# Optimization experiments

Hardware: AMD Instinct MI355X
Metric: run time of the kernel (lower is better)

The kernel has to match this reference:

```python
import jax, jax.numpy as jnp
import numpy as np

D = 512       # d_model
H = 8         # n_heads per pathway MHA
CTX_H = 2     # router context_attention heads
P = 16        # num_attention_pathways
K = 8         # top_k_pathways
B = 8
S = 1024
TEMP = 1.0
RH1, RH2 = 128, 64  # router hidden sizes


def mha(x, in_w, in_b, out_w, out_b, n_heads):
    """torch.nn.MultiheadAttention (batch_first, eval mode, no mask)."""
    b, s, d = x.shape
    dh = d // n_heads
    qkv = x @ in_w.T + in_b                      # [b,s,3d]
    q, k, v = jnp.split(qkv, 3, axis=-1)
    sh = lambda t: t.reshape(b, s, n_heads, dh).transpose(0, 2, 1, 3)
    q, k, v = sh(q), sh(k), sh(v)
    scale = 1.0 / float(np.sqrt(dh))
    attn = jax.nn.softmax(jnp.einsum('bhqd,bhkd->bhqk', q, k) * scale, axis=-1)
    o = jnp.einsum('bhqk,bhkd->bhqd', attn, v).transpose(0, 2, 1, 3).reshape(b, s, d)
    return o @ out_w.T + out_b


def setup_inputs() -> dict:
    key = jax.random.key(0)
    ks = jax.random.split(key, 16)
    w = 0.05  # weight init scale to keep attention logits sane
    return {
        'x': jax.random.normal(ks[0], (B, S, D), jnp.float32),
        'ctx_in_w': jax.random.normal(ks[1], (3 * D, D), jnp.float32) * w,
        'ctx_in_b': jnp.zeros((3 * D,), jnp.float32),
        'ctx_out_w': jax.random.normal(ks[2], (D, D), jnp.float32) * w,
        'ctx_out_b': jnp.zeros((D,), jnp.float32),
        'r_w1': jax.random.normal(ks[3], (RH1, D), jnp.float32) * w,
        'r_b1': jnp.zeros((RH1,), jnp.float32),
        'r_w2': jax.random.normal(ks[4], (RH2, RH1), jnp.float32) * w,
        'r_b2': jnp.zeros((RH2,), jnp.float32),
        'r_w3': jax.random.normal(ks[5], (P, RH2), jnp.float32) * w,
        'r_b3': jnp.zeros((P,), jnp.float32),
        'p_in_w': jax.random.normal(ks[6], (P, 3 * D, D), jnp.float32) * w,
        'p_in_b': jnp.zeros((P, 3 * D), jnp.float32),
        'p_out_w': jax.random.normal(ks[7], (P, D, D), jnp.float32) * w,
        'p_out_b': jnp.zeros((P, D), jnp.float32),
    }


def reference(x, ctx_in_w, ctx_in_b, ctx_out_w, ctx_out_b,
              r_w1, r_b1, r_w2, r_b2, r_w3, r_b3,
              p_in_w, p_in_b, p_out_w, p_out_b):
    b, s, d = x.shape
    # --- SemanticPathwayRouter ---
    attended = mha(x, ctx_in_w, ctx_in_b, ctx_out_w, ctx_out_b, CTX_H)
    h = jax.nn.relu(attended @ r_w1.T + r_b1)
    h = jax.nn.relu(h @ r_w2.T + r_b2)
    pathway_scores = h @ r_w3.T + r_b3            # [b,s,P]
    # --- GLBL load-balance loss (eval: no buffer updates) ---
    probs_lb = jax.nn.softmax(pathway_scores, axis=-1)
    freq = probs_lb.mean(axis=(0, 1))             # [P] (frequencies == avg scores)
    glbl_loss = P * jnp.sum(freq * freq)
    # --- top-k gating: softmax -> topk scatter -> renormalize ---
    probs = jax.nn.softmax(pathway_scores / TEMP, axis=-1)
    top_v, top_i = jax.lax.top_k(probs, K)        # [b,s,K]
    bi = jnp.arange(b)[:, None, None]
    si = jnp.arange(s)[None, :, None]
    weights = jnp.zeros_like(probs).at[bi, si, top_i].set(top_v)
    weights = weights / (weights.sum(axis=-1, keepdims=True) + 1e-8)
    # --- combine: weighted sum of P full-MHA experts (scan keeps memory low) ---
    wp = jnp.moveaxis(weights, -1, 0)             # [P,b,s]
    def step(acc, params):
        iw, ib, ow, ob, wk = params
        return acc + mha(x, iw, ib, ow, ob, H) * wk[..., None], None
    output, _ = jax.lax.scan(step, jnp.zeros_like(x),
                             (p_in_w, p_in_b, p_out_w, p_out_b, wp))
    return output, glbl_loss, weights
```

## Files before the change

### kernel.cpp

```cpp
#include <hip/hip_runtime.h>
#include <math.h>

#define TOKENS 8192
#define DM 512
#define TD 1536
#define SEQ 1024
#define NPATH 16
#define TOPK 8

typedef __bf16 bf16x8v __attribute__((ext_vector_type(8)));
typedef __bf16 bf16x4v __attribute__((ext_vector_type(4)));
typedef float f32x4v __attribute__((ext_vector_type(4)));

__device__ __forceinline__ void gload_lds16(const void* gp, unsigned lds_byte_off) {
    __builtin_amdgcn_global_load_lds(
        (const __attribute__((address_space(1))) unsigned int*)(uintptr_t)gp,
        (__attribute__((address_space(3))) unsigned int*)(uintptr_t)lds_byte_off,
        16, 0, 0);
}

__global__ __launch_bounds__(256)
void gemm_f32_nt(const float* __restrict__ A, const float* __restrict__ B,
                 const float* __restrict__ bias, float* __restrict__ C,
                 int M, int N, int K, int lda, int ldb, int ldc,
                 float alpha, int relu, int zmode)
{
    __shared__ float As[16][132];
    __shared__ float Bs[16][132];
    if (zmode == 1) {
        const int z = blockIdx.z, bb = z >> 1, hh = z & 1;
        A += (size_t)bb * SEQ * TD + hh * 256;
        B += (size_t)bb * SEQ * TD + 512 + hh * 256;
        C += (size_t)z * SEQ * SEQ;
    }
    const int tid = threadIdx.x;
    const int bm = blockIdx.y << 7, bn = blockIdx.x << 7;
    const int tx4 = (tid & 15) << 2, ty4 = ((tid >> 4) & 15) << 2;
    float acc[8][8] = {};
    for (int k0 = 0; k0 < K; k0 += 16) {
        __syncthreads();
#pragma unroll
        for (int it = 0; it < 2; ++it) {
            const int u = (it << 8) + tid;
            const int row = u >> 2, kc4 = (u & 3) << 2;
            const float4 av = *(const float4*)(A + (size_t)(bm + row) * lda + k0 + kc4);
            As[kc4 + 0][row] = av.x; As[kc4 + 1][row] = av.y;
            As[kc4 + 2][row] = av.z; As[kc4 + 3][row] = av.w;
            const float4 bv = *(const float4*)(B + (size_t)(bn + row) * ldb + k0 + kc4);
            Bs[kc4 + 0][row] = bv.x; Bs[kc4 + 1][row] = bv.y;
            Bs[kc4 + 2][row] = bv.z; Bs[kc4 + 3][row] = bv.w;
        }
        __syncthreads();
#pragma unroll
        for (int kk = 0; kk < 16; ++kk) {
            const float4 a0 = *(const float4*)&As[kk][ty4];
            const float4 a1 = *(const float4*)&As[kk][64 + ty4];
            const float4 b0 = *(const float4*)&Bs[kk][tx4];
            const float4 b1 = *(const float4*)&Bs[kk][64 + tx4];
            const float aa[8] = {a0.x, a0.y, a0.z, a0.w, a1.x, a1.y, a1.z, a1.w};
            const float bb[8] = {b0.x, b0.y, b0.z, b0.w, b1.x, b1.y, b1.z, b1.w};
#pragma unroll
            for (int i = 0; i < 8; ++i)
#pragma unroll
                for (int j = 0; j < 8; ++j)
                    acc[i][j] = fmaf(aa[i], bb[j], acc[i][j]);
        }
    }
    float bcol[8] = {};
    if (bias) {
        const float4 bL = *(const float4*)(bias + bn + tx4);
        const float4 bH = *(const float4*)(bias + bn + 64 + tx4);
        bcol[0] = bL.x; bcol[1] = bL.y; bcol[2] = bL.z; bcol[3] = bL.w;
        bcol[4] = bH.x; bcol[5] = bH.y; bcol[6] = bH.z; bcol[7] = bH.w;
    }
#pragma unroll
    for (int i = 0; i < 8; ++i) {
        const int row = bm + ((i < 4) ? (ty4 + i) : (64 + ty4 + i - 4));
        float* cp = C + (size_t)row * ldc + bn;
        float v[8];
#pragma unroll
        for (int j = 0; j < 8; ++j) {
            v[j] = alpha * acc[i][j] + bcol[j];
            if (relu) v[j] = fmaxf(v[j], 0.f);
        }
        *(float4*)(cp + tx4) = make_float4(v[0], v[1], v[2], v[3]);
        *(float4*)(cp + 64 + tx4) = make_float4(v[4], v[5], v[6], v[7]);
    }
}

__global__ __launch_bounds__(256)
void gemm_f32_pv(const float* __restrict__ Sb, const float* __restrict__ qkv,
                 float* __restrict__ obuf)
{
    __shared__ float As[16][132];
    __shared__ float Bs[16][128];
    const int z = blockIdx.z, bb = z >> 1, hh = z & 1;
    const float* A = Sb + (size_t)z * SEQ * SEQ;
    const float* B = qkv + (size_t)bb * SEQ * TD + 1024 + hh * 256;
    float* C = obuf + (size_t)bb * SEQ * 512 + hh * 256;
    const int tid = threadIdx.x;
    const int bm = blockIdx.y << 7, bn = blockIdx.x << 7;
    const int tx4 = (tid & 15) << 2, ty4 = ((tid >> 4) & 15) << 2;
    float acc[8][8] = {};
    for (int k0 = 0; k0 < SEQ; k0 += 16) {
        __syncthreads();
#pragma unroll
        for (int it = 0; it < 2; ++it) {
            const int u = (it << 8) + tid;
            const int row = u >> 2, kc4 = (u & 3) << 2;
            const float4 av = *(const float4*)(A + (size_t)(bm + row) * SEQ + k0 + kc4);
            As[kc4 + 0][row] = av.x; As[kc4 + 1][row] = av.y;
            As[kc4 + 2][row] = av.z; As[kc4 + 3][row] = av.w;
            const int krow = u >> 5, n4 = (u & 31) << 2;
            *(float4*)&Bs[krow][n4] = *(const float4*)(B + (size_t)(k0 + krow) * TD + bn + n4);
        }
        __syncthreads();
#pragma unroll
        for (int kk = 0; kk < 16; ++kk) {
            const float4 a0 = *(const float4*)&As[kk][ty4];
            const float4 a1 = *(const float4*)&As[kk][64 + ty4];
            const float4 b0 = *(const float4*)&Bs[kk][tx4];
            const float4 b1 = *(const float4*)&Bs[kk][64 + tx4];
            const float aa[8] = {a0.x, a0.y, a0.z, a0.w, a1.x, a1.y, a1.z, a1.w};
            const float bb[8] = {b0.x, b0.y, b0.z, b0.w, b1.x, b1.y, b1.z, b1.w};
#pragma unroll
            for (int i = 0; i < 8; ++i)
#pragma unroll
                for (int j = 0; j < 8; ++j)
                    acc[i][j] = fmaf(aa[i], bb[j], acc[i][j]);
        }
    }
#pragma unroll
    for (int i = 0; i < 8; ++i) {
        const int row = bm + ((i < 4) ? (ty4 + i) : (64 + ty4 + i - 4));
        float* cp = C + (size_t)row * 512 + bn;
        *(float4*)(cp + tx4) = make_float4(acc[i][0], acc[i][1], acc[i][2], acc[i][3]);
        *(float4*)(cp + 64 + tx4) = make_float4(acc[i][4], acc[i][5], acc[i][6], acc[i][7]);
    }
}

__global__ __launch_bounds__(256)
void softmax_rows(float* __restrict__ S_)
{
    const int row = blockIdx.x * 4 + (threadIdx.x >> 6);
    const int lane = threadIdx.x & 63;
    float* rp = S_ + (size_t)row * 1024 + lane * 16;
    float4 v[4];
#pragma unroll
    for (int i = 0; i < 4; ++i) v[i] = *(const float4*)(rp + i * 4);
    float mx = -INFINITY;
#pragma unroll
    for (int i = 0; i < 4; ++i)
        mx = fmaxf(mx, fmaxf(fmaxf(v[i].x, v[i].y), fmaxf(v[i].z, v[i].w)));
#pragma unroll
    for (int off = 1; off < 64; off <<= 1) mx = fmaxf(mx, __shfl_xor(mx, off));
    float sum = 0.f;
#pragma unroll
    for (int i = 0; i < 4; ++i) {
        v[i].x = __expf(v[i].x - mx); v[i].y = __expf(v[i].y - mx);
        v[i].z = __expf(v[i].z - mx); v[i].w = __expf(v[i].w - mx);
        sum += v[i].x + v[i].y + v[i].z + v[i].w;
    }
#pragma unroll
    for (int off = 1; off < 64; off <<= 1) sum += __shfl_xor(sum, off);
    const float inv = 1.f / sum;
#pragma unroll
    for (int i = 0; i < 4; ++i) {
        v[i].x *= inv; v[i].y *= inv; v[i].z *= inv; v[i].w *= inv;
        *(float4*)(rp + i * 4) = v[i];
    }
}

__global__ __launch_bounds__(256)
void gemm_f32(const float* __restrict__ A, const float* __restrict__ W,
              const float* __restrict__ bias, float* __restrict__ C,
              int M, int N, int K, int relu)
{
    __shared__ float As[16][64];
    __shared__ float Bs[16][64];
    const int bm = blockIdx.y << 6;
    const int bn = blockIdx.x << 6;
    const int tid = threadIdx.x;
    const int tx = tid & 15, ty = tid >> 4;
    const int lr = tid >> 2;
    const int lc = (tid & 3) << 2;
    float acc[4][4] = {};
    for (int k0 = 0; k0 < K; k0 += 16) {
        float4 av = *(const float4*)(A + (size_t)(bm + lr) * K + (k0 + lc));
        float4 bv = make_float4(0.f, 0.f, 0.f, 0.f);
        const int wr = bn + lr;
        if (wr < N) bv = *(const float4*)(W + (size_t)wr * K + (k0 + lc));
        __syncthreads();
        As[lc + 0][lr] = av.x; As[lc + 1][lr] = av.y;
        As[lc + 2][lr] = av.z; As[lc + 3][lr] = av.w;
        Bs[lc + 0][lr] = bv.x; Bs[lc + 1][lr] = bv.y;
        Bs[lc + 2][lr] = bv.z; Bs[lc + 3][lr] = bv.w;
        __syncthreads();
#pragma unroll
        for (int kk = 0; kk < 16; ++kk) {
            const float4 a4 = *(const float4*)(&As[kk][ty << 2]);
            const float4 b4 = *(const float4*)(&Bs[kk][tx << 2]);
            const float a[4] = {a4.x, a4.y, a4.z, a4.w};
            const float b[4] = {b4.x, b4.y, b4.z, b4.w};
#pragma unroll
            for (int i = 0; i < 4; ++i)
#pragma unroll
                for (int j = 0; j < 4; ++j)
                    acc[i][j] = fmaf(a[i], b[j], acc[i][j]);
        }
    }
#pragma unroll
    for (int i = 0; i < 4; ++i) {
        const int m = bm + (ty << 2) + i;
#pragma unroll
        for (int j = 0; j < 4; ++j) {
            const int n = bn + (tx << 2) + j;
            if (n < N) {
                float v = acc[i][j] + bias[n];
                if (relu) v = fmaxf(v, 0.f);
                C[(size_t)m * N + n] = v;
            }
        }
    }
}

template <int DH>
__global__ __launch_bounds__(256)
void flash_attn(const float* __restrict__ qkv, float* __restrict__ O,
                int H, float scale)
{
    constexpr int NU = DH / 64;
    __shared__ float Qs[32][DH + 4];
    __shared__ float Ks[32][DH + 4];
    __shared__ float Vs[32][DH + 4];
    __shared__ float Ps[32][33];
    const int tid = threadIdx.x;
    const int g2 = tid & 15;
    const int rs = tid >> 4;
    const int bh = blockIdx.y;
    const int b = bh / H, h = bh - b * H;
    const int rb = blockIdx.x << 5;
    const float* qb = qkv + (size_t)b * SEQ * TD + (size_t)h * DH;
    const float* kb = qb + DM;
    const float* vb = qb + 2 * DM;

    for (int idx = tid; idx < 32 * (DH / 4); idx += 256) {
        const int rr = idx / (DH / 4);
        const int dp = (idx - rr * (DH / 4)) << 2;
        float4 v = *(const float4*)(qb + (size_t)(rb + rr) * TD + dp);
        v.x *= scale; v.y *= scale; v.z *= scale; v.w *= scale;
        *(float4*)&Qs[rr][dp] = v;
    }
    float m0 = -INFINITY, m1 = -INFINITY, l0 = 0.f, l1 = 0.f;
    float4 o0[NU], o1[NU];
#pragma unroll
    for (int u = 0; u < NU; ++u) {
        o0[u] = make_float4(0.f, 0.f, 0.f, 0.f);
        o1[u] = make_float4(0.f, 0.f, 0.f, 0.f);
    }
    __syncthreads();

    for (int kt = 0; kt < SEQ; kt += 32) {
        for (int idx = tid; idx < 32 * (DH / 4); idx += 256) {
            const int rr = idx / (DH / 4);
            const int dp = (idx - rr * (DH / 4)) << 2;
            *(float4*)&Ks[rr][dp] = *(const float4*)(kb + (size_t)(kt + rr) * TD + dp);
            *(float4*)&Vs[rr][dp] = *(const float4*)(vb + (size_t)(kt + rr) * TD + dp);
        }
        __syncthreads();
        float s00 = 0.f, s01 = 0.f, s10 = 0.f, s11 = 0.f;
        const int cA = g2, cB = g2 + 16;
#pragma unroll 8
        for (int i = 0; i < DH; i += 4) {
            const float4 q0 = *(const float4*)&Qs[rs][i];
            const float4 q1 = *(const float4*)&Qs[rs + 16][i];
            const float4 k0 = *(const float4*)&Ks[cA][i];
            const float4 k1 = *(const float4*)&Ks[cB][i];
            s00 += q0.x * k0.x + q0.y * k0.y + q0.z * k0.z + q0.w * k0.w;
            s01 += q0.x * k1.x + q0.y * k1.y + q0.z * k1.z + q0.w * k1.w;
            s10 += q1.x * k0.x + q1.y * k0.y + q1.z * k0.z + q1.w * k0.w;
            s11 += q1.x * k1.x + q1.y * k1.y + q1.z * k1.z + q1.w * k1.w;
        }
        float ml0 = fmaxf(s00, s01), ml1 = fmaxf(s10, s11);
#pragma unroll
        for (int off = 1; off < 16; off <<= 1) {
            ml0 = fmaxf(ml0, __shfl_xor(ml0, off));
            ml1 = fmaxf(ml1, __shfl_xor(ml1, off));
        }
        const float n0 = fmaxf(m0, ml0), n1 = fmaxf(m1, ml1);
        const float f0 = __expf(m0 - n0), f1 = __expf(m1 - n1);
        const float p00 = __expf(s00 - n0), p01 = __expf(s01 - n0);
        const float p10 = __expf(s10 - n1), p11 = __expf(s11 - n1);
        float sum0 = p00 + p01, sum1 = p10 + p11;
#pragma unroll
        for (int off = 1; off < 16; off <<= 1) {
            sum0 += __shfl_xor(sum0, off);
            sum1 += __shfl_xor(sum1, off);
        }
        l0 = l0 * f0 + sum0; l1 = l1 * f1 + sum1;
        m0 = n0; m1 = n1;
#pragma unroll
        for (int u = 0; u < NU; ++u) {
            o0[u].x *= f0; o0[u].y *= f0; o0[u].z *= f0; o0[u].w *= f0;
            o1[u].x *= f1; o1[u].y *= f1; o1[u].z *= f1; o1[u].w *= f1;
        }
        Ps[rs][cA] = p00; Ps[rs][cB] = p01;
        Ps[rs + 16][cA] = p10; Ps[rs + 16][cB] = p11;
        __syncthreads();
#pragma unroll 4
        for (int c = 0; c < 32; ++c) {
            const float pv0 = Ps[rs][c];
            const float pv1 = Ps[rs + 16][c];
#pragma unroll
            for (int u = 0; u < NU; ++u) {
                const float4 v4 = *(const float4*)&Vs[c][(g2 << 2) + (u << 6)];
                o0[u].x = fmaf(pv0, v4.x, o0[u].x);
                o0[u].y = fmaf(pv0, v4.y, o0[u].y);
                o0[u].z = fmaf(pv0, v4.z, o0[u].z);
                o0[u].w = fmaf(pv0, v4.w, o0[u].w);
                o1[u].x = fmaf(pv1, v4.x, o1[u].x);
                o1[u].y = fmaf(pv1, v4.y, o1[u].y);
                o1[u].z = fmaf(pv1, v4.z, o1[u].z);
                o1[u].w = fmaf(pv1, v4.w, o1[u].w);
            }
        }
        __syncthreads();
    }
    const float i0 = 1.f / l0, i1 = 1.f / l1;
    float* ob0 = O + (size_t)b * SEQ * DM + (size_t)(rb + rs) * DM + h * DH;
    float* ob1 = ob0 + (size_t)16 * DM;
#pragma unroll
    for (int u = 0; u < NU; ++u) {
        float4 w0 = o0[u];
        w0.x *= i0; w0.y *= i0; w0.z *= i0; w0.w *= i0;
        *(float4*)(ob0 + (g2 << 2) + (u << 6)) = w0;
        float4 w1 = o1[u];
        w1.x *= i1; w1.y *= i1; w1.z *= i1; w1.w *= i1;
        *(float4*)(ob1 + (g2 << 2) + (u << 6)) = w1;
    }
}

__global__ __launch_bounds__(256)
void router_epilogue(const float* __restrict__ scores, float* __restrict__ freq,
                     float* __restrict__ weights)
{
    const int t = blockIdx.x * 256 + threadIdx.x;
    float s[NPATH];
#pragma unroll
    for (int i = 0; i < NPATH; ++i) s[i] = scores[(size_t)t * NPATH + i];
    float mx = s[0];
#pragma unroll
    for (int i = 1; i < NPATH; ++i) mx = fmaxf(mx, s[i]);
    float p[NPATH];
    float sum = 0.f;
#pragma unroll
    for (int i = 0; i < NPATH; ++i) { p[i] = expf(s[i] - mx); sum += p[i]; }
    const float inv = 1.f / sum;
#pragma unroll
    for (int i = 0; i < NPATH; ++i) p[i] *= inv;
#pragma unroll
    for (int i = 0; i < NPATH; ++i) {
        float v = p[i];
        for (int off = 32; off >= 1; off >>= 1) v += __shfl_xor(v, off);
        if ((threadIdx.x & 63) == 0) atomicAdd(&freq[i], v);
    }
    unsigned used = 0u;
    float topv[TOPK];
    int topi[TOPK];
    float wsum = 0.f;
#pragma unroll
    for (int k = 0; k < TOPK; ++k) {
        float best = -1.f; int bi = 0;
#pragma unroll
        for (int i = 0; i < NPATH; ++i) {
            if (!((used >> i) & 1u) && p[i] > best) { best = p[i]; bi = i; }
        }
        used |= 1u << bi;
        topv[k] = best; topi[k] = bi;
        wsum += best;
    }
    const float winv = 1.f / (wsum + 1e-8f);
    float w[NPATH];
#pragma unroll
    for (int i = 0; i < NPATH; ++i) w[i] = 0.f;
#pragma unroll
    for (int k = 0; k < TOPK; ++k) w[topi[k]] = topv[k] * winv;
#pragma unroll
    for (int i = 0; i < NPATH; ++i) weights[(size_t)t * NPATH + i] = w[i];
}

__global__ void glbl_loss_kernel(const float* __restrict__ freq, float* __restrict__ out)
{
    if (threadIdx.x == 0 && blockIdx.x == 0) {
        float acc = 0.f;
        for (int i = 0; i < NPATH; ++i) {
            const float f = freq[i] * (1.f / (float)TOKENS);
            acc += f * f;
        }
        out[0] = (float)NPATH * acc;
    }
}

__global__ __launch_bounds__(256)
void cast_f32_bf16(const float* __restrict__ src, __bf16* __restrict__ dst, int n)
{
    const int i = (blockIdx.x * 256 + threadIdx.x) * 4;
    if (i < n) {
        const float4 v = *(const float4*)(src + i);
        bf16x4v o;
        o[0] = (__bf16)v.x; o[1] = (__bf16)v.y; o[2] = (__bf16)v.z; o[3] = (__bf16)v.w;
        *(bf16x4v*)(dst + i) = o;
    }
}

__global__ __launch_bounds__(256)
void gemm_bf16_qkv(const __bf16* __restrict__ A, const __bf16* __restrict__ B,
                   const float* __restrict__ bias, __bf16* __restrict__ C,
                   int N, int K)
{
    __shared__ __attribute__((aligned(16))) __bf16 As[128 * 32];
    __shared__ __attribute__((aligned(16))) __bf16 Bs[128 * 32];
    const int tid = threadIdx.x;
    const int l = tid & 63, w = tid >> 6;
    const int wr = w >> 1, wc = w & 1;
    const int a16 = l & 15, g = l >> 4;
    const int bm = blockIdx.y << 7, bn = blockIdx.x << 7;
    const unsigned asA = (unsigned)(uintptr_t)(void*)&As[0];
    const unsigned asB = (unsigned)(uintptr_t)(void*)&Bs[0];

    f32x4v acc[4][4] = {};
    for (int k0 = 0; k0 < K; k0 += 32) {
        __syncthreads();
#pragma unroll
        for (int it = 0; it < 2; ++it) {
            const int u = it * 256 + tid;
            const int row = u >> 2, cc = u & 3;
            const unsigned dst = (unsigned)((it * 256 + w * 64) * 16);
            gload_lds16(A + (size_t)(bm + row) * K + k0 + cc * 8, asA + dst);
            gload_lds16(B + (size_t)(bn + row) * K + k0 + cc * 8, asB + dst);
        }
        __syncthreads();
        bf16x8v af[4], bf[4];
#pragma unroll
        for (int m = 0; m < 4; ++m)
            af[m] = *(const bf16x8v*)&As[(wr * 64 + m * 16 + a16) * 32 + g * 8];
#pragma unroll
        for (int n = 0; n < 4; ++n)
            bf[n] = *(const bf16x8v*)&Bs[(wc * 64 + n * 16 + a16) * 32 + g * 8];
#pragma unroll
        for (int m = 0; m < 4; ++m)
#pragma unroll
            for (int n = 0; n < 4; ++n)
                acc[m][n] = __builtin_amdgcn_mfma_f32_16x16x32_bf16(af[m], bf[n], acc[m][n], 0, 0, 0);
    }
#pragma unroll
    for (int n = 0; n < 4; ++n) {
        const int col = bn + wc * 64 + n * 16 + a16;
        const float bv = bias[col];
        const float sc = (col < DM) ? 0.125f : 1.0f;
#pragma unroll
        for (int m = 0; m < 4; ++m) {
            const int row0 = bm + wr * 64 + m * 16 + g * 4;
#pragma unroll
            for (int r = 0; r < 4; ++r)
                C[(size_t)(row0 + r) * N + col] = (__bf16)((acc[m][n][r] + bv) * sc);
        }
    }
}

__global__ __launch_bounds__(256)
void gemm_bf16_out(const __bf16* __restrict__ A, const __bf16* __restrict__ B,
                   const float* __restrict__ bias, const float* __restrict__ wts,
                   float* __restrict__ out, int path, int first)
{
    __shared__ __attribute__((aligned(16))) __bf16 As[128 * 32];
    __shared__ __attribute__((aligned(16))) __bf16 Bs[128 * 32];
    const int tid = threadIdx.x;
    const int l = tid & 63, w = tid >> 6;
    const int wr = w >> 1, wc = w & 1;
    const int a16 = l & 15, g = l >> 4;
    const int bm = blockIdx.y << 7, bn = blockIdx.x << 7;
    const unsigned asA = (unsigned)(uintptr_t)(void*)&As[0];
    const unsigned asB = (unsigned)(uintptr_t)(void*)&Bs[0];

    f32x4v acc[4][4] = {};
    for (int k0 = 0; k0 < DM; k0 += 32) {
        __syncthreads();
#pragma unroll
        for (int it = 0; it < 2; ++it) {
            const int u = it * 256 + tid;
            const int row = u >> 2, cc = u & 3;
            const unsigned dst = (unsigned)((it * 256 + w * 64) * 16);
            gload_lds16(A + (size_t)(bm + row) * DM + k0 + cc * 8, asA + dst);
            gload_lds16(B + (size_t)(bn + row) * DM + k0 + cc * 8, asB + dst);
        }
        __syncthreads();
        bf16x8v af[4], bf[4];
#pragma unroll
        for (int m = 0; m < 4; ++m)
            af[m] = *(const bf16x8v*)&As[(wr * 64 + m * 16 + a16) * 32 + g * 8];
#pragma unroll
        for (int n = 0; n < 4; ++n)
            bf[n] = *(const bf16x8v*)&Bs[(wc * 64 + n * 16 + a16) * 32 + g * 8];
#pragma unroll
        for (int m = 0; m < 4; ++m)
#pragma unroll
            for (int n = 0; n < 4; ++n)
                acc[m][n] = __builtin_amdgcn_mfma_f32_16x16x32_bf16(af[m], bf[n], acc[m][n], 0, 0, 0);
    }
#pragma unroll
    for (int m = 0; m < 4; ++m) {
        const int row0 = bm + wr * 64 + m * 16 + g * 4;
#pragma unroll
        for (int r = 0; r < 4; ++r) {
            const int row = row0 + r;
            const float wk = wts[(size_t)row * NPATH + path];
#pragma unroll
            for (int n = 0; n < 4; ++n) {
                const int col = bn + wc * 64 + n * 16 + a16;
                const float v = (acc[m][n][r] + bias[col]) * wk;
                const size_t oi = (size_t)row * DM + col;
                if (first) out[oi] = v; else out[oi] += v;
            }
        }
    }
}

__global__ __launch_bounds__(256)
void attn_bf16(const __bf16* __restrict__ qkv, __bf16* __restrict__ O)
{
    __shared__ __attribute__((aligned(16))) __bf16 Ks[64 * 72];
    __shared__ __attribute__((aligned(16))) __bf16 Vt[64 * 72];
    __shared__ __attribute__((aligned(16))) __bf16 Pq[4][16 * 72];
    const int tid = threadIdx.x;
    const int l = tid & 63, w = tid >> 6;
    const int a = l & 15, g = l >> 4;
    const int bh = blockIdx.y;
    const int b = bh >> 3, h = bh & 7;
    const int qb = blockIdx.x << 6;
    const size_t base = (size_t)b * SEQ * TD;

    bf16x8v qf[2];
    {
        const int qrow = qb + w * 16 + a;
        const __bf16* qp = qkv + base + (size_t)qrow * TD + h * 64 + g * 8;
        qf[0] = *(const bf16x8v*)qp;
        qf[1] = *(const bf16x8v*)(qp + 32);
    }
    float m_ = -INFINITY, l_ = 0.f;
    f32x4v o_[4] = {};
    __bf16* pw = &Pq[w][0];

    for (int kt = 0; kt < SEQ; kt += 64) {
#pragma unroll
        for (int it = 0; it < 2; ++it) {
            const int u = it * 256 + tid;
            const int kr = u >> 3, c8 = u & 7;
            const __bf16* kp = qkv + base + (size_t)(kt + kr) * TD + DM + h * 64 + c8 * 8;
            const bf16x8v kv = *(const bf16x8v*)kp;
            *(bf16x8v*)&Ks[kr * 72 + c8 * 8] = kv;
            const bf16x8v vv = *(const bf16x8v*)(kp + DM);
            const int swzg = ((kr >> 3) ^ c8) & 7;
#pragma unroll
            for (int j = 0; j < 8; ++j)
                Vt[(c8 * 8 + j) * 72 + swzg * 8 + (kr & 7)] = vv[j];
        }
        __syncthreads();

        f32x4v s[4] = {};
#pragma unroll
        for (int kc = 0; kc < 4; ++kc) {
            const bf16x8v kf0 = *(const bf16x8v*)&Ks[(kc * 16 + a) * 72 + g * 8];
            const bf16x8v kf1 = *(const bf16x8v*)&Ks[(kc * 16 + a) * 72 + 32 + g * 8];
            s[kc] = __builtin_amdgcn_mfma_f32_16x16x32_bf16(kf0, qf[0], s[kc], 0, 0, 0);
            s[kc] = __builtin_amdgcn_mfma_f32_16x16x32_bf16(kf1, qf[1], s[kc], 0, 0, 0);
        }

        float pmax = s[0][0];
#pragma unroll
        for (int kc = 0; kc < 4; ++kc)
#pragma unroll
            for (int r = 0; r < 4; ++r) pmax = fmaxf(pmax, s[kc][r]);
        pmax = fmaxf(pmax, __shfl_xor(pmax, 16));
        pmax = fmaxf(pmax, __shfl_xor(pmax, 32));

        if (__any(pmax > m_ + 8.f)) {
            const float nm = fmaxf(m_, pmax);
            const float f = __expf(m_ - nm);
            m_ = nm;
            l_ *= f;
#pragma unroll
            for (int r = 0; r < 4; ++r) {
                const float fr = __shfl(f, 4 * g + r);
#pragma unroll
                for (int dc = 0; dc < 4; ++dc) o_[dc][r] *= fr;
            }
        }
        float p[4][4];
        float lsum = 0.f;
#pragma unroll
        for (int kc = 0; kc < 4; ++kc)
#pragma unroll
            for (int r = 0; r < 4; ++r) {
                p[kc][r] = __expf(s[kc][r] - m_);
                lsum += p[kc][r];
            }
        lsum += __shfl_xor(lsum, 16);
        lsum += __shfl_xor(lsum, 32);
        l_ += lsum;

#pragma unroll
        for (int kc = 0; kc < 4; ++kc) {
            bf16x4v pk;
            pk[0] = (__bf16)p[kc][0]; pk[1] = (__bf16)p[kc][1];
            pk[2] = (__bf16)p[kc][2]; pk[3] = (__bf16)p[kc][3];
            *(bf16x4v*)&pw[a * 72 + kc * 16 + g * 4] = pk;
        }
        asm volatile("s_waitcnt lgkmcnt(0)" ::: "memory");

#pragma unroll
        for (int dc = 0; dc < 4; ++dc) {
            const int vrow = dc * 16 + a;
#pragma unroll
            for (int kh = 0; kh < 2; ++kh) {
                const bf16x8v pa = *(const bf16x8v*)&pw[a * 72 + kh * 32 + g * 8];
                const bf16x8v vf = *(const bf16x8v*)&Vt[vrow * 72 + ((((kh << 2) + g) ^ ((vrow >> 3) & 7)) & 7) * 8];
                o_[dc] = __builtin_amdgcn_mfma_f32_16x16x32_bf16(pa, vf, o_[dc], 0, 0, 0);
            }
        }
        __syncthreads();
    }

    float linv[4];
#pragma unroll
    for (int r = 0; r < 4; ++r) linv[r] = 1.f / __shfl(l_, 4 * g + r);
    const int row0 = qb + w * 16 + g * 4;
#pragma unroll
    for (int dc = 0; dc < 4; ++dc)
#pragma unroll
        for (int r = 0; r < 4; ++r)
            O[(size_t)(b * SEQ + row0 + r) * DM + h * 64 + dc * 16 + a] = (__bf16)(o_[dc][r] * linv[r]);
}

extern "C" void kernel_launch(void* const* d_in, const int* in_sizes, int n_in,
                              void* d_out, int out_size, void* d_ws, size_t ws_size,
                              hipStream_t stream)
{
    const float* x         = (const float*)d_in[0];
    const float* ctx_in_w  = (const float*)d_in[1];
    const float* ctx_in_b  = (const float*)d_in[2];
    const float* ctx_out_w = (const float*)d_in[3];
    const float* ctx_out_b = (const float*)d_in[4];
    const float* r_w1      = (const float*)d_in[5];
    const float* r_b1      = (const float*)d_in[6];
    const float* r_w2      = (const float*)d_in[7];
    const float* r_b2      = (const float*)d_in[8];
    const float* r_w3      = (const float*)d_in[9];
    const float* r_b3      = (const float*)d_in[10];
    const float* p_in_w    = (const float*)d_in[11];
    const float* p_in_b    = (const float*)d_in[12];
    const float* p_out_w   = (const float*)d_in[13];
    const float* p_out_b   = (const float*)d_in[14];

    float* out  = (float*)d_out;
    float* loss = out + (size_t)TOKENS * DM;
    float* wts  = loss + 1;

    float* F = (float*)d_ws;
    float* qkvbuf   = F;
    float* obuf     = F + 12582912;
    float* attended = F;
    float* h1       = F + 4194304;
    float* h2       = F + 5242880;
    float* scores   = F + 5767168;
    float* freq     = F + 5898240;

    const int M = TOKENS;
    dim3 blk(256);
    const bool big = ws_size >= (size_t)134217728;

    hipMemsetAsync(freq, 0, NPATH * sizeof(float), stream);
    gemm_f32_nt<<<dim3(TD / 128, M / 128), blk, 0, stream>>>(
        x, ctx_in_w, ctx_in_b, qkvbuf, M, TD, DM, DM, DM, TD, 1.f, 0, 0);
    if (big) {
        float* Sbuf = F + 16777216;
        gemm_f32_nt<<<dim3(8, 8, 16), blk, 0, stream>>>(
            qkvbuf, qkvbuf, nullptr, Sbuf, SEQ, SEQ, 256, TD, TD, SEQ, 0.0625f, 0, 1);
        softmax_rows<<<dim3(16 * SEQ / 4), blk, 0, stream>>>(Sbuf);
        gemm_f32_pv<<<dim3(2, 8, 16), blk, 0, stream>>>(Sbuf, qkvbuf, obuf);
    } else {
        flash_attn<256><<<dim3(SEQ / 32, 8 * 2), blk, 0, stream>>>(qkvbuf, obuf, 2, 1.f / 16.f);
    }
    gemm_f32_nt<<<dim3(DM / 128, M / 128), blk, 0, stream>>>(
        obuf, ctx_out_w, ctx_out_b, attended, M, DM, DM, DM, DM, DM, 1.f, 0, 0);
    gemm_f32_nt<<<dim3(1, M / 128), blk, 0, stream>>>(
        attended, r_w1, r_b1, h1, M, 128, DM, DM, DM, 128, 1.f, 1, 0);
    gemm_f32<<<dim3(1, M / 64), blk, 0, stream>>>(h1, r_w2, r_b2, h2, M, 64, 128, 1);
    gemm_f32<<<dim3(1, M / 64), blk, 0, stream>>>(h2, r_w3, r_b3, scores, M, NPATH, 64, 0);
    router_epilogue<<<dim3(TOKENS / 256), blk, 0, stream>>>(scores, freq, wts);
    glbl_loss_kernel<<<dim3(1), dim3(64), 0, stream>>>(freq, loss);

    if (big) {
        __bf16* xb       = (__bf16*)F;
        __bf16* qkv_b    = (__bf16*)(F + 2097152);
        __bf16* obuf_b   = (__bf16*)(F + 8388608);
        __bf16* wqkv_all = (__bf16*)(F + 10485760);
        __bf16* wout_all = (__bf16*)(F + 16777216);
        cast_f32_bf16<<<dim3(TOKENS * DM / 4 / 256), blk, 0, stream>>>(x, xb, TOKENS * DM);
        cast_f32_bf16<<<dim3(NPATH * TD * DM / 4 / 256), blk, 0, stream>>>(
            p_in_w, wqkv_all, NPATH * TD * DM);
        cast_f32_bf16<<<dim3(NPATH * DM * DM / 4 / 256), blk, 0, stream>>>(
            p_out_w, wout_all, NPATH * DM * DM);
        for (int p = 0; p < NPATH; ++p) {
            gemm_bf16_qkv<<<dim3(TD / 128, M / 128), blk, 0, stream>>>(
                xb, wqkv_all + (size_t)p * TD * DM, p_in_b + (size_t)p * TD, qkv_b, TD, DM);
            attn_bf16<<<dim3(SEQ / 64, 64), blk, 0, stream>>>(qkv_b, obuf_b);
            gemm_bf16_out<<<dim3(DM / 128, M / 128), blk, 0, stream>>>(
                obuf_b, wout_all + (size_t)p * DM * DM, p_out_b + (size_t)p * DM, wts, out, p, p == 0);
        }
    } else {
        __bf16* xb     = (__bf16*)F;
        __bf16* qkv_b  = (__bf16*)(F + 6000000);
        __bf16* obuf_b = (__bf16*)(F + 12582912);
        __bf16* wqkv_b = (__bf16*)(F + 12582912 + 2100000);
        __bf16* wout_b = (__bf16*)(F + 12582912 + 2500000);
        cast_f32_bf16<<<dim3(TOKENS * DM / 4 / 256), blk, 0, stream>>>(x, xb, TOKENS * DM);
        for (int p = 0; p < NPATH; ++p) {
            cast_f32_bf16<<<dim3(TD * DM / 4 / 256), blk, 0, stream>>>(
                p_in_w + (size_t)p * TD * DM, wqkv_b, TD * DM);
            cast_f32_bf16<<<dim3(DM * DM / 4 / 256), blk, 0, stream>>>(
                p_out_w + (size_t)p * DM * DM, wout_b, DM * DM);
            gemm_bf16_qkv<<<dim3(TD / 128, M / 128), blk, 0, stream>>>(
                xb, wqkv_b, p_in_b + (size_t)p * TD, qkv_b, TD, DM);
            attn_bf16<<<dim3(SEQ / 64, 64), blk, 0, stream>>>(qkv_b, obuf_b);
            gemm_bf16_out<<<dim3(DM / 128, M / 128), blk, 0, stream>>>(
                obuf_b, wout_b, p_out_b + (size_t)p * DM, wts, out, p, p == 0);
        }
    }
}
```

Measured before the change: 2.358 ms.

## Add 256x128 fp32 GEMM tile, vectorize V transpose, set MFMA priority

Adds a new fp32 GEMM kernel with a 256x128 block tile (16x8 outputs per thread) and uses it for the router's context QKV, out-projection and first MLP layer. The goal is more data reuse per LDS load and fewer blocks. The pathway attention kernel now builds the transposed V tile by packing two rows into 32-bit LDS stores instead of scalar bf16 stores, and raises wave priority around the MFMA sections. Workspace offsets are reshuffled. The 128 accumulators per thread raise register pressure and may lower occupancy.

```diff
diff --git a/kernel.cpp b/kernel.cpp
--- a/kernel.cpp
+++ b/kernel.cpp
@@ -11,12 +11,83 @@
 typedef __bf16 bf16x8v __attribute__((ext_vector_type(8)));
 typedef __bf16 bf16x4v __attribute__((ext_vector_type(4)));
 typedef float f32x4v __attribute__((ext_vector_type(4)));
+typedef unsigned short u16x8 __attribute__((ext_vector_type(8)));
 
 __device__ __forceinline__ void gload_lds16(const void* gp, unsigned lds_byte_off) {
     __builtin_amdgcn_global_load_lds(
         (const __attribute__((address_space(1))) unsigned int*)(uintptr_t)gp,
         (__attribute__((address_space(3))) unsigned int*)(uintptr_t)lds_byte_off,
         16, 0, 0);
+}
+
+__global__ __launch_bounds__(256)
+void gemm_f32_nt2(const float* __restrict__ A, const float* __restrict__ B,
+                  const float* __restrict__ bias, float* __restrict__ C,
+                  int K, int lda, int ldb, int ldc, int relu)
+{
+    __shared__ float As[16][260];
+    __shared__ float Bs[16][132];
+    const int tid = threadIdx.x;
+    const int bm = blockIdx.y << 8, bn = blockIdx.x << 7;
+    const int tx4 = (tid & 15) << 2, ty4 = ((tid >> 4) & 15) << 2;
+    float acc[16][8] = {};
+    for (int k0 = 0; k0 < K; k0 += 16) {
+        __syncthreads();
+#pragma unroll
+        for (int it = 0; it < 4; ++it) {
+            const int u = (it << 8) + tid;
+            const int row = u >> 2, kc4 = (u & 3) << 2;
+            const float4 av = *(const float4*)(A + (size_t)(bm + row) * lda + k0 + kc4);
+            As[kc4 + 0][row] = av.x; As[kc4 + 1][row] = av.y;
+            As[kc4 + 2][row] = av.z; As[kc4 + 3][row] = av.w;
+        }
+#pragma unroll
+        for (int it = 0; it < 2; ++it) {
+            const int u = (it << 8) + tid;
+            const int row = u >> 2, kc4 = (u & 3) << 2;
+            const float4 bv = *(const float4*)(B + (size_t)(bn + row) * ldb + k0 + kc4);
+            Bs[kc4 + 0][row] = bv.x; Bs[kc4 + 1][row] = bv.y;
+            Bs[kc4 + 2][row] = bv.z; Bs[kc4 + 3][row] = bv.w;
+        }
+        __syncthreads();
+#pragma unroll
+        for (int kk = 0; kk < 16; ++kk) {
+            const float4 A0 = *(const float4*)&As[kk][ty4];
+            const float4 A1 = *(const float4*)&As[kk][64 + ty4];
+            const float4 A2 = *(const float4*)&As[kk][128 + ty4];
+            const float4 A3 = *(const float4*)&As[kk][192 + ty4];
+            const float4 B0 = *(const float4*)&Bs[kk][tx4];
+            const float4 B1 = *(const float4*)&Bs[kk][64 + tx4];
+            const float aa[16] = {A0.x, A0.y, A0.z, A0.w, A1.x, A1.y, A1.z, A1.w,
+                                  A2.x, A2.y, A2.z, A2.w, A3.x, A3.y, A3.z, A3.w};
+            const float bb[8] = {B0.x, B0.y, B0.z, B0.w, B1.x, B1.y, B1.z, B1.w};
+#pragma unroll
+            for (int i = 0; i < 16; ++i)
+#pragma unroll
+                for (int j = 0; j < 8; ++j)
+                    acc[i][j] = fmaf(aa[i], bb[j], acc[i][j]);
+        }
+    }
+    float bcol[8];
+    {
+        const float4 bL = *(const float4*)(bias + bn + tx4);
+        const float4 bH = *(const float4*)(bias + bn + 64 + tx4);
+        bcol[0] = bL.x; bcol[1] = bL.y; bcol[2] = bL.z; bcol[3] = bL.w;
+        bcol[4] = bH.x; bcol[5] = bH.y; bcol[6] = bH.z; bcol[7] = bH.w;
+    }
+#pragma unroll
+    for (int i = 0; i < 16; ++i) {
+        const int row = bm + (i >> 2) * 64 + ty4 + (i & 3);
+        float* cp = C + (size_t)row * ldc + bn;
+        float v[8];
+#pragma unroll
+        for (int j = 0; j < 8; ++j) {
+            v[j] = acc[i][j] + bcol[j];
+            if (relu) v[j] = fmaxf(v[j], 0.f);
+        }
+        *(float4*)(cp + tx4) = make_float4(v[0], v[1], v[2], v[3]);
+        *(float4*)(cp + 64 + tx4) = make_float4(v[4], v[5], v[6], v[7]);
+    }
 }
 
 __global__ __launch_bounds__(256)
@@ -550,6 +621,9 @@
     float m_ = -INFINITY, l_ = 0.f;
     f32x4v o_[4] = {};
     __bf16* pw = &Pq[w][0];
+    const int c8v = tid & 7;
+    const int pr  = tid >> 3;
+    const int vcol8 = (pr >> 2) ^ c8v;
 
     for (int kt = 0; kt < SEQ; kt += 64) {
 #pragma unroll
@@ -557,17 +631,22 @@
             const int u = it * 256 + tid;
             const int kr = u >> 3, c8 = u & 7;
             const __bf16* kp = qkv + base + (size_t)(kt + kr) * TD + DM + h * 64 + c8 * 8;
-            const bf16x8v kv = *(const bf16x8v*)kp;
-            *(bf16x8v*)&Ks[kr * 72 + c8 * 8] = kv;
-            const bf16x8v vv = *(const bf16x8v*)(kp + DM);
-            const int swzg = ((kr >> 3) ^ c8) & 7;
-#pragma unroll
-            for (int j = 0; j < 8; ++j)
-                Vt[(c8 * 8 + j) * 72 + swzg * 8 + (kr & 7)] = vv[j];
+            *(bf16x8v*)&Ks[kr * 72 + c8 * 8] = *(const bf16x8v*)kp;
+        }
+        {
+            const __bf16* vp = qkv + base + (size_t)(kt + 2 * pr) * TD + 2 * DM + h * 64 + c8v * 8;
+            const u16x8 v0 = __builtin_bit_cast(u16x8, *(const bf16x8v*)vp);
+            const u16x8 v1 = __builtin_bit_cast(u16x8, *(const bf16x8v*)(vp + TD));
+#pragma unroll
+            for (int j = 0; j < 8; ++j) {
+                const unsigned pk = (unsigned)v0[j] | ((unsigned)v1[j] << 16);
+                *(unsigned*)&Vt[(c8v * 8 + j) * 72 + vcol8 * 8 + (pr & 3) * 2] = pk;
+            }
         }
         __syncthreads();
 
         f32x4v s[4] = {};
+        __builtin_amdgcn_s_setprio(1);
 #pragma unroll
         for (int kc = 0; kc < 4; ++kc) {
             const bf16x8v kf0 = *(const bf16x8v*)&Ks[(kc * 16 + a) * 72 + g * 8];
@@ -575,6 +654,7 @@
             s[kc] = __builtin_amdgcn_mfma_f32_16x16x32_bf16(kf0, qf[0], s[kc], 0, 0, 0);
             s[kc] = __builtin_amdgcn_mfma_f32_16x16x32_bf16(kf1, qf[1], s[kc], 0, 0, 0);
         }
+        __builtin_amdgcn_s_setprio(0);
 
         float pmax = s[0][0];
 #pragma unroll
@@ -618,6 +698,7 @@
         }
         asm volatile("s_waitcnt lgkmcnt(0)" ::: "memory");
 
+        __builtin_amdgcn_s_setprio(1);
 #pragma unroll
         for (int dc = 0; dc < 4; ++dc) {
             const int vrow = dc * 16 + a;
@@ -628,6 +709,7 @@
                 o_[dc] = __builtin_amdgcn_mfma_f32_16x16x32_bf16(pa, vf, o_[dc], 0, 0, 0);
             }
         }
+        __builtin_amdgcn_s_setprio(0);
         __syncthreads();
     }
 
@@ -680,8 +762,8 @@
     const bool big = ws_size >= (size_t)134217728;
 
     hipMemsetAsync(freq, 0, NPATH * sizeof(float), stream);
-    gemm_f32_nt<<<dim3(TD / 128, M / 128), blk, 0, stream>>>(
-        x, ctx_in_w, ctx_in_b, qkvbuf, M, TD, DM, DM, DM, TD, 1.f, 0, 0);
+    gemm_f32_nt2<<<dim3(TD / 128, M / 256), blk, 0, stream>>>(
+        x, ctx_in_w, ctx_in_b, qkvbuf, DM, DM, DM, TD, 0);
     if (big) {
         float* Sbuf = F + 16777216;
         gemm_f32_nt<<<dim3(8, 8, 16), blk, 0, stream>>>(
@@ -691,10 +773,10 @@
     } else {
         flash_attn<256><<<dim3(SEQ / 32, 8 * 2), blk, 0, stream>>>(qkvbuf, obuf, 2, 1.f / 16.f);
     }
-    gemm_f32_nt<<<dim3(DM / 128, M / 128), blk, 0, stream>>>(
-        obuf, ctx_out_w, ctx_out_b, attended, M, DM, DM, DM, DM, DM, 1.f, 0, 0);
-    gemm_f32_nt<<<dim3(1, M / 128), blk, 0, stream>>>(
-        attended, r_w1, r_b1, h1, M, 128, DM, DM, DM, 128, 1.f, 1, 0);
+    gemm_f32_nt2<<<dim3(DM / 128, M / 256), blk, 0, stream>>>(
+        obuf, ctx_out_w, ctx_out_b, attended, DM, DM, DM, DM, 0);
+    gemm_f32_nt2<<<dim3(1, M / 256), blk, 0, stream>>>(
+        attended, r_w1, r_b1, h1, DM, DM, DM, 128, 1);
     gemm_f32<<<dim3(1, M / 64), blk, 0, stream>>>(h1, r_w2, r_b2, h2, M, 64, 128, 1);
     gemm_f32<<<dim3(1, M / 64), blk, 0, stream>>>(h2, r_w3, r_b3, scores, M, NPATH, 64, 0);
     router_epilogue<<<dim3(TOKENS / 256), blk, 0, stream>>>(scores, freq, wts);
@@ -704,8 +786,8 @@
         __bf16* xb       = (__bf16*)F;
         __bf16* qkv_b    = (__bf16*)(F + 2097152);
         __bf16* obuf_b   = (__bf16*)(F + 8388608);
-        __bf16* wqkv_all = (__bf16*)(F + 10485760);
-        __bf16* wout_all = (__bf16*)(F + 16777216);
+        __bf16* wqkv_all = (__bf16*)(F + 16777216);
+        __bf16* wout_all = (__bf16*)(F + 23068672);
         cast_f32_bf16<<<dim3(TOKENS * DM / 4 / 256), blk, 0, stream>>>(x, xb, TOKENS * DM);
         cast_f32_bf16<<<dim3(NPATH * TD * DM / 4 / 256), blk, 0, stream>>>(
             p_in_w, wqkv_all, NPATH * TD * DM);
@@ -720,10 +802,10 @@
         }
     } else {
         __bf16* xb     = (__bf16*)F;
-        __bf16* qkv_b  = (__bf16*)(F + 6000000);
-        __bf16* obuf_b = (__bf16*)(F + 12582912);
-        __bf16* wqkv_b = (__bf16*)(F + 12582912 + 2100000);
-        __bf16* wout_b = (__bf16*)(F + 12582912 + 2500000);
+        __bf16* qkv_b  = (__bf16*)(F + 2097152);
+        __bf16* obuf_b = (__bf16*)(F + 8388608);
+        __bf16* wqkv_b = (__bf16*)(F + 12582912);
+        __bf16* wout_b = (__bf16*)(F + 12976128);
         cast_f32_bf16<<<dim3(TOKENS * DM / 4 / 256), blk, 0, stream>>>(x, xb, TOKENS * DM);
         for (int p = 0; p < NPATH; ++p) {
             cast_f32_bf16<<<dim3(TD * DM / 4 / 256), blk, 0, stream>>>(
```

After: 2.453 ms. +4.0%, slower.
